# Performance work log

Hardware: AMD Instinct MI355X
Metric: run time of the kernel (lower is better)

Reference implementation:

```python
import jax, jax.numpy as jnp
import numpy as np

BS, N, GD, ND, ED = 8, 256, 64, 64, 32


def setup_inputs() -> dict:
    key = jax.random.key(0)
    ks = jax.random.split(key, 9)
    p = lambda k, shape: (jax.random.normal(k, shape, dtype=jnp.float32) * 0.05)
    return {
        "u": jax.random.normal(ks[0], (BS, GD), dtype=jnp.float32),
        "V": jax.random.normal(ks[1], (BS, N, ND), dtype=jnp.float32),
        "A": jax.random.normal(ks[2], (BS, N, N, ED), dtype=jnp.float32),
        "W_A": p(ks[3], (ED + 2 * ND + GD, ED)),   # f_A_nn
        "b_A": p(ks[4], (ED,)),
        "W_v": p(ks[5], (ED + ND + GD, ND)),        # f_v_nn
        "b_v": p(ks[6], (ND,)),
        "W_u": p(ks[7], (ED + ND + GD, GD)),        # f_u_nn
        "b_u": p(ks[8], (GD,)),
    }


def reference(u, V, A, W_A, b_A, W_v, b_v, W_u, b_u):
    bs, n, nd = V.shape
    ed = A.shape[-1]
    gd = u.shape[-1]
    # f_A: torch concat order is [A, V_j, V_i, u] where x[b,i,j] uses
    # V_j = V[b,j] (from V.unsqueeze(1).expand) and V_i = V[b,i] (its transpose).
    # Split the linear to avoid materializing the [bs,n,n,224] concat tensor.
    Wa_e = W_A[:ed]
    Wa_vj = W_A[ed:ed + nd]
    Wa_vi = W_A[ed + nd:ed + 2 * nd]
    Wa_u = W_A[ed + 2 * nd:]
    A_prime = jax.nn.relu(
        jnp.einsum("bije,eo->bijo", A, Wa_e)
        + (V @ Wa_vj)[:, None, :, :]   # broadcast over i
        + (V @ Wa_vi)[:, :, None, :]   # broadcast over j
        + (u @ Wa_u)[:, None, None, :]
        + b_A
    )  # [bs, n, n, ed]
    # rho_A_v: mean over dim 1
    A_agg_by_node = A_prime.mean(axis=1)  # [bs, n, ed]
    # f_v
    u_b = jnp.broadcast_to(u[:, None, :], (bs, n, gd))
    xv = jnp.concatenate([A_agg_by_node, V, u_b], axis=-1)
    V_prime = jax.nn.relu(xv @ W_v + b_v)  # [bs, n, nd]
    # rho_A_u, rho_v_u
    A_agg = A_prime.mean(axis=(1, 2))  # [bs, ed]
    v_agg = V_prime.mean(axis=1)       # [bs, nd]
    # f_u
    xu = jnp.concatenate([A_agg, v_agg, u], axis=-1)
    u_prime = jax.nn.relu(xu @ W_u + b_u)  # [bs, gd]
    return (u_prime, V_prime, A_prime)
```

## Files before the change

kernel.cpp:

```cpp
#include <hip/hip_runtime.h>
#include <stdint.h>

#define BS 8
#define NN 256
#define GD 64
#define ND 64
#define ED 32

#define GLOBAL_AS __attribute__((address_space(1)))
#define LDS_AS    __attribute__((address_space(3)))

__global__ __launch_bounds__(256) void k1_proj(
        const float* __restrict__ u, const float* __restrict__ V,
        const float* __restrict__ W_A, const float* __restrict__ b_A,
        float* __restrict__ vj, float* __restrict__ vi, float* __restrict__ up,
        float* __restrict__ colsum) {
    __shared__ float W2[2 * ND][ED];
    __shared__ float Vt[32][ND];
    int t   = threadIdx.x;
    int blk = blockIdx.x;
    int bn0 = blk * 32;
    {
        float4* cz = (float4*)(colsum + blk * 1024);
        cz[t] = make_float4(0.f, 0.f, 0.f, 0.f);
    }
    {
        const float4* src = (const float4*)(W_A + ED * ED);
        float4* dst = (float4*)&W2[0][0];
#pragma unroll
        for (int r = 0; r < 4; ++r) dst[r * 256 + t] = src[r * 256 + t];
    }
    {
        const float4* src = (const float4*)(V + (size_t)bn0 * ND);
        float4* dst = (float4*)&Vt[0][0];
        dst[t]       = src[t];
        dst[256 + t] = src[256 + t];
    }
    __syncthreads();
    int rq  = t >> 6;
    int oo  = t & 63;
    int mat = oo >> 5;
    int o   = oo & 31;
#pragma unroll 2
    for (int p = 0; p < 8; ++p) {
        int rl = p * 4 + rq;
        int bn = bn0 + rl;
        float d0 = 0.f, d1 = 0.f, d2 = 0.f, d3 = 0.f;
#pragma unroll
        for (int k = 0; k < ND; k += 4) {
            d0 = fmaf(Vt[rl][k + 0], W2[mat * ND + k + 0][o], d0);
            d1 = fmaf(Vt[rl][k + 1], W2[mat * ND + k + 1][o], d1);
            d2 = fmaf(Vt[rl][k + 2], W2[mat * ND + k + 2][o], d2);
            d3 = fmaf(Vt[rl][k + 3], W2[mat * ND + k + 3][o], d3);
        }
        float acc = (d0 + d1) + (d2 + d3);
        if (mat == 0) vj[bn * ED + o] = acc;
        else          vi[bn * ED + o] = acc;
    }
    if (blk < 8 && t < 32) {
        float a2 = b_A[t];
#pragma unroll 8
        for (int k = 0; k < GD; ++k)
            a2 = fmaf(u[blk * GD + k], W_A[(ED + 2 * ND + k) * ED + t], a2);
        up[blk * ED + t] = a2;
    }
}

__global__ __launch_bounds__(256) void k2_main(
        const float* __restrict__ A, const float* __restrict__ W_A,
        const float* __restrict__ vj, const float* __restrict__ vi,
        const float* __restrict__ up,
        float* __restrict__ Aprime, float* __restrict__ colsum) {
    __shared__ float tile[16][8][ED];
    __shared__ float vit[16][ED];
    int bid = blockIdx.x;
    int b   = bid >> 9;
    int it  = (bid >> 5) & 15;
    int jc  = bid & 31;
    int t    = threadIdx.x;
    int lane = t & 63;
    int wv   = t >> 6;
    int i0 = it * 16;
    int j0 = jc * 8;

    const float* Asrc = A + ((size_t)(b * NN + i0) * NN + j0) * ED;
#pragma unroll
    for (int r = 0; r < 4; ++r) {
        int il = r * 4 + wv;
        const float* g = Asrc + (size_t)il * NN * ED + lane * 4;
        __builtin_amdgcn_global_load_lds((const GLOBAL_AS void*)g,
                                         (LDS_AS void*)&tile[il][0][0], 16, 0, 0);
    }
    {
        const float* vsrc = vi + (size_t)(b * NN + i0) * ED;
        ((float*)vit)[t]       = vsrc[t];
        ((float*)vit)[t + 256] = vsrc[t + 256];
    }
    int jloc = t >> 5;
    int o    = t & 31;
    int j    = j0 + jloc;
    float w_[ED];
#pragma unroll
    for (int e = 0; e < ED; ++e) w_[e] = W_A[e * ED + o];
    float cj = vj[(b * NN + j) * ED + o] + up[b * ED + o];

    __syncthreads();

    float colacc = 0.f;
    float* Pb = Aprime + ((size_t)(b * NN + i0) * NN + j) * ED + o;
#pragma unroll 2
    for (int ii = 0; ii < 16; ++ii) {
        const float4* lr = (const float4*)(&tile[ii][jloc][0]);
        float d0 = 0.f, d1 = 0.f, d2 = 0.f, d3 = 0.f;
#pragma unroll
        for (int q = 0; q < 8; ++q) {
            float4 f = lr[q];
            d0 = fmaf(f.x, w_[4 * q + 0], d0);
            d1 = fmaf(f.y, w_[4 * q + 1], d1);
            d2 = fmaf(f.z, w_[4 * q + 2], d2);
            d3 = fmaf(f.w, w_[4 * q + 3], d3);
        }
        float v = (d0 + d1) + (d2 + d3) + cj + vit[ii][o];
        v = fmaxf(v, 0.f);
        Pb[(size_t)ii * NN * ED] = v;
        colacc += v;
    }
    atomicAdd(&colsum[(b * NN + j) * ED + o], colacc);
}

__global__ __launch_bounds__(256) void k3_vprime(
        const float* __restrict__ V, const float* __restrict__ u,
        const float* __restrict__ W_v, const float* __restrict__ b_v,
        const float* __restrict__ colsum, float* __restrict__ Vprime) {
    __shared__ float Wv[ED + ND + GD][ND];
    __shared__ float xv[16][ED + ND + GD];
    int t = threadIdx.x;
    {
        const float4* src = (const float4*)W_v;
        float4* dst = (float4*)&Wv[0][0];
#pragma unroll
        for (int r = 0; r < 10; ++r) dst[r * 256 + t] = src[r * 256 + t];
    }
    int bn0 = blockIdx.x * 16;
    int d  = t & 63;
    int rq = t >> 6;
#pragma unroll
    for (int p = 0; p < 4; ++p) {
        int rl = p * 4 + rq;
        int bn = bn0 + rl;
        int b  = bn >> 8;
        if (d < 32) xv[rl][d] = colsum[bn * ED + d] * (1.f / 256.f);
        xv[rl][ED + d]      = V[(size_t)bn * ND + d];
        xv[rl][ED + ND + d] = u[b * GD + d];
    }
    __syncthreads();
#pragma unroll 2
    for (int p = 0; p < 4; ++p) {
        int rl = p * 4 + rq;
        int bn = bn0 + rl;
        float acc = b_v[d];
#pragma unroll 8
        for (int k = 0; k < ED + ND + GD; ++k)
            acc = fmaf(xv[rl][k], Wv[k][d], acc);
        Vprime[(size_t)bn * ND + d] = fmaxf(acc, 0.f);
    }
}

__global__ __launch_bounds__(256) void k4_uprime(
        const float* __restrict__ u,
        const float* __restrict__ W_u, const float* __restrict__ b_u,
        const float* __restrict__ colsum, const float* __restrict__ Vprime,
        float* __restrict__ uprime) {
    int b = blockIdx.x;
    int t = threadIdx.x;
    __shared__ float vpart[4][ND];
    __shared__ float apart[8][ED];
    __shared__ float xu[ED + ND + GD];
    {
        int d = t & 63, g = t >> 6;
        float s = 0.f;
        for (int n = g; n < NN; n += 4)
            s += Vprime[(size_t)(b * NN + n) * ND + d];
        vpart[g][d] = s;
    }
    {
        int o = t & 31, g = t >> 5;
        float s = 0.f;
        for (int n = g; n < NN; n += 8)
            s += colsum[(b * NN + n) * ED + o];
        apart[g][o] = s;
    }
    __syncthreads();
    if (t < 32) {
        float s = 0.f;
#pragma unroll
        for (int g = 0; g < 8; ++g) s += apart[g][t];
        xu[t] = s * (1.f / 65536.f);
    }
    if (t < 64) {
        xu[ED + t]      = (vpart[0][t] + vpart[1][t] + vpart[2][t] + vpart[3][t]) * (1.f / 256.f);
        xu[ED + ND + t] = u[b * GD + t];
    }
    __syncthreads();
    if (t < 64) {
        float acc = b_u[t];
#pragma unroll 8
        for (int k = 0; k < ED + ND + GD; ++k)
            acc = fmaf(xu[k], W_u[k * GD + t], acc);
        uprime[b * GD + t] = fmaxf(acc, 0.f);
    }
}

extern "C" void kernel_launch(void* const* d_in, const int* in_sizes, int n_in,
                              void* d_out, int out_size, void* d_ws, size_t ws_size,
                              hipStream_t stream) {
    const float* u   = (const float*)d_in[0];
    const float* V   = (const float*)d_in[1];
    const float* A   = (const float*)d_in[2];
    const float* W_A = (const float*)d_in[3];
    const float* b_A = (const float*)d_in[4];
    const float* W_v = (const float*)d_in[5];
    const float* b_v = (const float*)d_in[6];
    const float* W_u = (const float*)d_in[7];
    const float* b_u = (const float*)d_in[8];

    float* out    = (float*)d_out;
    float* uprime = out;
    float* Vprime = out + BS * GD;
    float* Aprime = out + BS * GD + BS * NN * ND;

    float* ws     = (float*)d_ws;
    float* vj     = ws;
    float* vi     = vj + BS * NN * ED;
    float* up     = vi + BS * NN * ED;
    float* colsum = up + BS * ED;

    hipLaunchKernelGGL(k1_proj, dim3(64), dim3(256), 0, stream,
                       u, V, W_A, b_A, vj, vi, up, colsum);
    hipLaunchKernelGGL(k2_main, dim3(BS * 16 * 32), dim3(256), 0, stream,
                       A, W_A, vj, vi, up, Aprime, colsum);
    hipLaunchKernelGGL(k3_vprime, dim3(128), dim3(256), 0, stream,
                       V, u, W_v, b_v, colsum, Vprime);
    hipLaunchKernelGGL(k4_uprime, dim3(BS), dim3(256), 0, stream,
                       u, W_u, b_u, colsum, Vprime, uprime);
}
```

Measured before the change: 186.3 us.

## Fuse u-prime reductions into V-prime kernel and use nontemporal A-prime stores

The per-batch reductions of V_prime and the column sums move out of the final kernel into the V_prime kernel. There they are accumulated through block-level shared reductions and atomics into small aggregate buffers, which the first kernel now zeroes. The final kernel becomes a 64-thread linear layer that no longer rereads V_prime and colsum. Separately, the large A_prime output is written with nontemporal stores to reduce cache pollution. The atomic float adds make the summation order nondeterministic.

```diff
diff --git a/kernel.cpp b/kernel.cpp
--- a/kernel.cpp
+++ b/kernel.cpp
@@ -21,8 +21,9 @@
     int blk = blockIdx.x;
     int bn0 = blk * 32;
     {
-        float4* cz = (float4*)(colsum + blk * 1024);
-        cz[t] = make_float4(0.f, 0.f, 0.f, 0.f);
+        float4 z4 = make_float4(0.f, 0.f, 0.f, 0.f);
+        ((float4*)colsum)[blk * 256 + t] = z4;
+        if (blk == 0 && t < 192) ((float4*)(colsum + BS * NN * ED))[t] = z4;
     }
     {
         const float4* src = (const float4*)(W_A + ED * ED);
@@ -122,7 +123,7 @@
         }
         float v = (d0 + d1) + (d2 + d3) + cj + vit[ii][o];
         v = fmaxf(v, 0.f);
-        Pb[(size_t)ii * NN * ED] = v;
+        __builtin_nontemporal_store(v, &Pb[(size_t)ii * NN * ED]);
         colacc += v;
     }
     atomicAdd(&colsum[(b * NN + j) * ED + o], colacc);
@@ -131,9 +132,12 @@
 __global__ __launch_bounds__(256) void k3_vprime(
         const float* __restrict__ V, const float* __restrict__ u,
         const float* __restrict__ W_v, const float* __restrict__ b_v,
-        const float* __restrict__ colsum, float* __restrict__ Vprime) {
+        const float* __restrict__ colsum, float* __restrict__ Vprime,
+        float* __restrict__ vagg, float* __restrict__ aagg) {
     __shared__ float Wv[ED + ND + GD][ND];
-    __shared__ float xv[16][ED + ND + GD];
+    __shared__ float xv[16][ED + ND + GD + 1];
+    __shared__ float vred[4][ND];
+    __shared__ float ared[4][ED];
     int t = threadIdx.x;
     {
         const float4* src = (const float4*)W_v;
@@ -142,73 +146,63 @@
         for (int r = 0; r < 10; ++r) dst[r * 256 + t] = src[r * 256 + t];
     }
     int bn0 = blockIdx.x * 16;
+    int b   = bn0 >> 8;
     int d  = t & 63;
     int rq = t >> 6;
 #pragma unroll
     for (int p = 0; p < 4; ++p) {
         int rl = p * 4 + rq;
         int bn = bn0 + rl;
-        int b  = bn >> 8;
         if (d < 32) xv[rl][d] = colsum[bn * ED + d] * (1.f / 256.f);
         xv[rl][ED + d]      = V[(size_t)bn * ND + d];
         xv[rl][ED + ND + d] = u[b * GD + d];
     }
     __syncthreads();
+    float vsum = 0.f;
 #pragma unroll 2
     for (int p = 0; p < 4; ++p) {
         int rl = p * 4 + rq;
-        int bn = bn0 + rl;
         float acc = b_v[d];
 #pragma unroll 8
         for (int k = 0; k < ED + ND + GD; ++k)
             acc = fmaf(xv[rl][k], Wv[k][d], acc);
-        Vprime[(size_t)bn * ND + d] = fmaxf(acc, 0.f);
-    }
-}
-
-__global__ __launch_bounds__(256) void k4_uprime(
+        acc = fmaxf(acc, 0.f);
+        Vprime[(size_t)(bn0 + rl) * ND + d] = acc;
+        vsum += acc;
+    }
+    vred[rq][d] = vsum;
+    if (d < 32) {
+        float asum = xv[rq][d] + xv[4 + rq][d] + xv[8 + rq][d] + xv[12 + rq][d];
+        ared[rq][d] = asum;
+    }
+    __syncthreads();
+    if (t < 64) {
+        atomicAdd(&vagg[b * ND + t],
+                  vred[0][t] + vred[1][t] + vred[2][t] + vred[3][t]);
+    } else if (t < 96) {
+        int o = t - 64;
+        atomicAdd(&aagg[b * ED + o],
+                  ared[0][o] + ared[1][o] + ared[2][o] + ared[3][o]);
+    }
+}
+
+__global__ __launch_bounds__(64) void k4_uprime(
         const float* __restrict__ u,
         const float* __restrict__ W_u, const float* __restrict__ b_u,
-        const float* __restrict__ colsum, const float* __restrict__ Vprime,
+        const float* __restrict__ vagg, const float* __restrict__ aagg,
         float* __restrict__ uprime) {
     int b = blockIdx.x;
     int t = threadIdx.x;
-    __shared__ float vpart[4][ND];
-    __shared__ float apart[8][ED];
     __shared__ float xu[ED + ND + GD];
-    {
-        int d = t & 63, g = t >> 6;
-        float s = 0.f;
-        for (int n = g; n < NN; n += 4)
-            s += Vprime[(size_t)(b * NN + n) * ND + d];
-        vpart[g][d] = s;
-    }
-    {
-        int o = t & 31, g = t >> 5;
-        float s = 0.f;
-        for (int n = g; n < NN; n += 8)
-            s += colsum[(b * NN + n) * ED + o];
-        apart[g][o] = s;
-    }
-    __syncthreads();
-    if (t < 32) {
-        float s = 0.f;
-#pragma unroll
-        for (int g = 0; g < 8; ++g) s += apart[g][t];
-        xu[t] = s * (1.f / 65536.f);
-    }
-    if (t < 64) {
-        xu[ED + t]      = (vpart[0][t] + vpart[1][t] + vpart[2][t] + vpart[3][t]) * (1.f / 256.f);
-        xu[ED + ND + t] = u[b * GD + t];
-    }
-    __syncthreads();
-    if (t < 64) {
-        float acc = b_u[t];
+    if (t < 32) xu[t] = aagg[b * ED + t] * (1.f / 256.f);
+    xu[ED + t]      = vagg[b * ND + t] * (1.f / 256.f);
+    xu[ED + ND + t] = u[b * GD + t];
+    __syncthreads();
+    float acc = b_u[t];
 #pragma unroll 8
-        for (int k = 0; k < ED + ND + GD; ++k)
-            acc = fmaf(xu[k], W_u[k * GD + t], acc);
-        uprime[b * GD + t] = fmaxf(acc, 0.f);
-    }
+    for (int k = 0; k < ED + ND + GD; ++k)
+        acc = fmaf(xu[k], W_u[k * GD + t], acc);
+    uprime[b * GD + t] = fmaxf(acc, 0.f);
 }
 
 extern "C" void kernel_launch(void* const* d_in, const int* in_sizes, int n_in,
@@ -234,13 +228,15 @@
     float* vi     = vj + BS * NN * ED;
     float* up     = vi + BS * NN * ED;
     float* colsum = up + BS * ED;
+    float* vagg   = colsum + BS * NN * ED;
+    float* aagg   = vagg + BS * ND;
 
     hipLaunchKernelGGL(k1_proj, dim3(64), dim3(256), 0, stream,
                        u, V, W_A, b_A, vj, vi, up, colsum);
-    hipLaunchKernelGGL(k2_main, dim3(BS * 16 * 32), dim3(256), 0, stream,
+    hipLaunchKernelGGL(k2_main, dim3(4096), dim3(256), 0, stream,
                        A, W_A, vj, vi, up, Aprime, colsum);
     hipLaunchKernelGGL(k3_vprime, dim3(128), dim3(256), 0, stream,
-                       V, u, W_v, b_v, colsum, Vprime);
-    hipLaunchKernelGGL(k4_uprime, dim3(BS), dim3(256), 0, stream,
-                       u, W_u, b_u, colsum, Vprime, uprime);
-}
+                       V, u, W_v, b_v, colsum, Vprime, vagg, aagg);
+    hipLaunchKernelGGL(k4_uprime, dim3(BS), dim3(64), 0, stream,
+                       u, W_u, b_u, vagg, aagg, uprime);
+}
```

New measurement: 162.8 us. -12.6%, faster.
